# Kernel tuning notes

Measured on AMD Instinct MI355X. Metric: run time of the kernel, lower is better.

The kernel has to match this reference:

```python
import jax, jax.numpy as jnp
import numpy as np
import math
from jax import lax

B, T, D, K, H, MLP_DIM, WIN = 4, 2048, 1024, 64, 4, 4096, 128
KH = K // H          # eigenstates per head
HD = D // H          # attention head dim


def layer_norm(x, g, b, eps=1e-5):
    mu = jnp.mean(x, axis=-1, keepdims=True)
    var = jnp.mean(jnp.square(x - mu), axis=-1, keepdims=True)
    return (x - mu) * lax.rsqrt(var + eps) * g + b


def setup_inputs() -> dict:
    key = jax.random.key(0)
    ks = jax.random.split(key, 16)
    s = 0.02
    # layer_idx=1, n_layers=6 -> depth_ratio=0.2, decay_center=-1.7
    return {
        "x": jax.random.normal(ks[0], (B, T, D), jnp.float32),
        "prev_eigenstates": jax.random.normal(ks[1], (B, T, 2 * K), jnp.float32),
        "norm1_g": jnp.ones((D,), jnp.float32),
        "norm1_b": jnp.zeros((D,), jnp.float32),
        "in_proj_w": jax.random.normal(ks[2], (2 * K, D), jnp.float32) * s,
        "memory_gate": jnp.array(-3.0, jnp.float32),
        "memory_proj_w": jnp.eye(2 * K, dtype=jnp.float32),
        "log_decay": jax.random.uniform(ks[3], (K,), jnp.float32, -2.7, -1.2),
        "frequency": jnp.linspace(0.0, 2 * math.pi * (1 - 1 / K), K, dtype=jnp.float32),
        "coupling": jnp.tile(jnp.eye(KH, dtype=jnp.float32), (H, 1, 1))
                    + 0.01 * jax.random.normal(ks[4], (H, KH, KH), jnp.float32) / math.sqrt(KH),
        "main_gate_w": jax.random.normal(ks[5], (D, D), jnp.float32) * s,
        "main_gate_b": jnp.full((D,), -2.0, jnp.float32),
        "out_proj_w": jax.random.normal(ks[6], (D, 2 * K), jnp.float32) * s,
        "attn_norm_g": jnp.ones((D,), jnp.float32),
        "attn_norm_b": jnp.zeros((D,), jnp.float32),
        "attn_in_w": jax.random.normal(ks[7], (3 * D, D), jnp.float32) * s,
        "attn_in_b": jnp.zeros((3 * D,), jnp.float32),
        "attn_out_w": jax.random.normal(ks[8], (D, D), jnp.float32) * s,
        "attn_out_b": jnp.zeros((D,), jnp.float32),
        "norm2_g": jnp.ones((D,), jnp.float32),
        "norm2_b": jnp.zeros((D,), jnp.float32),
        "mlp_w1": jax.random.normal(ks[9], (MLP_DIM, D), jnp.float32) * s,
        "mlp_b1": jnp.zeros((MLP_DIM,), jnp.float32),
        "mlp_w2": jax.random.normal(ks[10], (D, MLP_DIM), jnp.float32) * s,
        "mlp_b2": jnp.zeros((D,), jnp.float32),
    }


def eigenstate_fft(log_decay, frequency, beta_r, beta_i):
    # diagonal complex SSM recurrence: c_t = lam * c_{t-1} + beta_t
    lam = jnp.exp(log_decay)
    lr = lam * jnp.cos(frequency)   # (K,)
    li = lam * jnp.sin(frequency)
    br = jnp.transpose(beta_r, (1, 0, 2))  # (T,B,K)
    bi = jnp.transpose(beta_i, (1, 0, 2))

    def step(carry, inp):
        sr, si = carry
        xr, xi = inp
        nr = lr * sr - li * si + xr
        ni = lr * si + li * sr + xi
        return (nr, ni), (nr, ni)

    init = (jnp.zeros(br.shape[1:], br.dtype), jnp.zeros(bi.shape[1:], bi.dtype))
    _, (cr, ci) = lax.scan(step, init, (br, bi))
    return jnp.transpose(cr, (1, 0, 2)), jnp.transpose(ci, (1, 0, 2))


def reference(x, prev_eigenstates, norm1_g, norm1_b, in_proj_w, memory_gate,
              memory_proj_w, log_decay, frequency, coupling, main_gate_w,
              main_gate_b, out_proj_w, attn_norm_g, attn_norm_b, attn_in_w,
              attn_in_b, attn_out_w, attn_out_b, norm2_g, norm2_b,
              mlp_w1, mlp_b1, mlp_w2, mlp_b2):
    b, t, d = x.shape
    residual = x
    x_norm = layer_norm(x, norm1_g, norm1_b)

    beta = jnp.einsum('btd,kd->btk', x_norm, in_proj_w)        # (B,T,2K)
    beta_r, beta_i = jnp.split(beta, 2, axis=-1)

    # cross-layer memory
    mg = jax.nn.sigmoid(memory_gate)
    prev = jnp.einsum('btk,jk->btj', prev_eigenstates, memory_proj_w)
    pr, pi = jnp.split(prev, 2, axis=-1)
    beta_r = beta_r + mg * pr
    beta_i = beta_i + mg * pi

    c_r, c_i = eigenstate_fft(log_decay, frequency, beta_r, beta_i)  # (B,T,K)

    # per-head coupling
    c_r_h = c_r.reshape(b, t, H, KH)
    c_i_h = c_i.reshape(b, t, H, KH)
    c_r = jnp.einsum('hjk,bthk->bthj', coupling, c_r_h).reshape(b, t, K)
    c_i = jnp.einsum('hjk,bthk->bthj', coupling, c_i_h).reshape(b, t, K)
    eigenstates_out = jnp.concatenate([c_r, c_i], axis=-1)     # (B,T,2K)

    h = jnp.einsum('btk,dk->btd', eigenstates_out, out_proj_w)
    # spectral gate (band gates computed in torch are unused in the output)
    main_g = jax.nn.sigmoid(jnp.einsum('btd,ed->bte', x_norm, main_gate_w) + main_gate_b)
    h = main_g * h
    x = residual + h

    # sliding-window attention (dense masked MHA, as in the source)
    attn_in = layer_norm(x, attn_norm_g, attn_norm_b)
    qkv = jnp.einsum('btd,ed->bte', attn_in, attn_in_w) + attn_in_b
    q, k_, v = jnp.split(qkv, 3, axis=-1)
    q = q.reshape(b, t, H, HD).transpose(0, 2, 1, 3)           # (B,H,T,hd)
    k_ = k_.reshape(b, t, H, HD).transpose(0, 2, 1, 3)
    v = v.reshape(b, t, H, HD).transpose(0, 2, 1, 3)
    scale = 1.0 / math.sqrt(HD)
    scores = jnp.einsum('bhqd,bhkd->bhqk', q, k_) * scale
    idx = jnp.arange(t)
    diff = idx[:, None] - idx[None, :]
    allowed = (diff >= 0) & (diff <= WIN)                      # True = attend
    scores = jnp.where(allowed, scores, jnp.finfo(scores.dtype).min)
    attn = jax.nn.softmax(scores, axis=-1)
    ao = jnp.einsum('bhqk,bhkd->bhqd', attn, v)
    ao = ao.transpose(0, 2, 1, 3).reshape(b, t, d)
    ao = jnp.einsum('btd,ed->bte', ao, attn_out_w) + attn_out_b
    x = x + ao

    # MLP
    x2 = layer_norm(x, norm2_g, norm2_b)
    m = jax.nn.silu(jnp.einsum('btd,md->btm', x2, mlp_w1) + mlp_b1)
    m = jnp.einsum('btm,dm->btd', m, mlp_w2) + mlp_b2
    x = x + m
    return (x, eigenstates_out)
```

## Files before the change

kernel.cpp:

```cpp
#include <hip/hip_runtime.h>


typedef __bf16 bf16_t;
typedef bf16_t bf16x8 __attribute__((ext_vector_type(8)));
typedef bf16_t bf16x4 __attribute__((ext_vector_type(4)));
typedef float  f32x4  __attribute__((ext_vector_type(4)));

#define Tc   2048
#define Dc   1024
#define BTc  8192
#define K2c  128
#define MLPc 4096

struct ConvSeg { const float* src; bf16_t* dst; int n; };
struct ConvArgs { ConvSeg s[9]; };

__global__ __launch_bounds__(256) void convert_kernel(ConvArgs a) {
    ConvSeg sg = a.s[blockIdx.y];
    int i = (blockIdx.x * 256 + threadIdx.x) * 4;
    if (i >= sg.n) return;
    float4 v = *(const float4*)(sg.src + i);
    bf16x4 o;
    o[0] = (bf16_t)v.x; o[1] = (bf16_t)v.y; o[2] = (bf16_t)v.z; o[3] = (bf16_t)v.w;
    *(bf16x4*)(sg.dst + i) = o;
}

__global__ __launch_bounds__(256) void ln_kernel(const float* __restrict__ x,
                                                 const float* __restrict__ g,
                                                 const float* __restrict__ bb,
                                                 bf16_t* __restrict__ out) {
    int row = blockIdx.x;
    int tid = threadIdx.x;
    float4 v = ((const float4*)(x + (size_t)row * Dc))[tid];
    float s  = v.x + v.y + v.z + v.w;
    float ss = v.x * v.x + v.y * v.y + v.z * v.z + v.w * v.w;
#pragma unroll
    for (int d = 32; d > 0; d >>= 1) {
        s  += __shfl_down(s, d);
        ss += __shfl_down(ss, d);
    }
    __shared__ float red[8];
    int wv = tid >> 6;
    if ((tid & 63) == 0) { red[wv] = s; red[4 + wv] = ss; }
    __syncthreads();
    s  = red[0] + red[1] + red[2] + red[3];
    ss = red[4] + red[5] + red[6] + red[7];
    float mean = s * (1.0f / Dc);
    float var  = ss * (1.0f / Dc) - mean * mean;
    float rstd = rsqrtf(var + 1e-5f);
    float4 g4 = ((const float4*)g)[tid];
    float4 b4 = ((const float4*)bb)[tid];
    bf16x4 o;
    o[0] = (bf16_t)((v.x - mean) * rstd * g4.x + b4.x);
    o[1] = (bf16_t)((v.y - mean) * rstd * g4.y + b4.y);
    o[2] = (bf16_t)((v.z - mean) * rstd * g4.z + b4.z);
    o[3] = (bf16_t)((v.w - mean) * rstd * g4.w + b4.w);
    *(bf16x4*)(out + (size_t)row * Dc + tid * 4) = o;
}

#define BM 128
#define BN 128
#define BK 32

struct EpiParams {
    const float* bias;
    float*       fout;
    const float* fin;
    bf16_t*      bout;
    bf16_t*      q; bf16_t* k; bf16_t* v;
    const float* hbuf;
};

#define GLOAD_LDS(g, l)                                                        \
    __builtin_amdgcn_global_load_lds(                                          \
        (const __attribute__((address_space(1))) unsigned int*)(g),            \
        (__attribute__((address_space(3))) unsigned int*)(l), 16, 0, 0)

template <int EPI>
__global__ __launch_bounds__(256) void gemm_tiled(const bf16_t* __restrict__ A,
                                                  const bf16_t* __restrict__ W,
                                                  int M, int N, int K,
                                                  EpiParams ep) {
    __shared__ bf16_t As[BM * BK];
    __shared__ bf16_t Bs[BN * BK];

    int tid = threadIdx.x;
    int wv = tid >> 6, lane = tid & 63;
    int lane16 = lane & 15, quad = lane >> 4;
    int nbn = N / BN;
    int bm = blockIdx.x / nbn, bn = blockIdx.x % nbn;
    int m0 = bm * BM, n0 = bn * BN;
    int wm = (wv >> 1) * 64, wn = (wv & 1) * 64;

    int lrow = lane >> 2;
    int lcol = (lane & 3) * 8;
    const bf16_t* ga = A + (size_t)(m0 + wv * 16 + lrow) * K + lcol;
    const bf16_t* gb = W + (size_t)(n0 + wv * 16 + lrow) * K + lcol;
    size_t gstep64 = (size_t)64 * K;
    bf16_t* la0 = &As[(wv * 16) * BK];
    bf16_t* la1 = &As[(64 + wv * 16) * BK];
    bf16_t* lb0 = &Bs[(wv * 16) * BK];
    bf16_t* lb1 = &Bs[(64 + wv * 16) * BK];

    f32x4 zz = {0.f, 0.f, 0.f, 0.f};
    f32x4 acc[4][4];
#pragma unroll
    for (int mi = 0; mi < 4; mi++)
#pragma unroll
        for (int ni = 0; ni < 4; ni++) acc[mi][ni] = zz;

    for (int k0 = 0; k0 < K; k0 += BK) {
        GLOAD_LDS(ga + k0, la0);
        GLOAD_LDS(ga + k0 + gstep64, la1);
        GLOAD_LDS(gb + k0, lb0);
        GLOAD_LDS(gb + k0 + gstep64, lb1);
        __syncthreads();
        bf16x8 af[4], bfr[4];
#pragma unroll
        for (int mi = 0; mi < 4; mi++)
            af[mi] = *(const bf16x8*)&As[(wm + mi * 16 + lane16) * BK + quad * 8];
#pragma unroll
        for (int ni = 0; ni < 4; ni++)
            bfr[ni] = *(const bf16x8*)&Bs[(wn + ni * 16 + lane16) * BK + quad * 8];
#pragma unroll
        for (int mi = 0; mi < 4; mi++)
#pragma unroll
            for (int ni = 0; ni < 4; ni++)
                acc[mi][ni] = __builtin_amdgcn_mfma_f32_16x16x32_bf16(
                    af[mi], bfr[ni], acc[mi][ni], 0, 0, 0);
        __syncthreads();
    }

#pragma unroll
    for (int mi = 0; mi < 4; mi++)
#pragma unroll
        for (int ni = 0; ni < 4; ni++)
#pragma unroll
            for (int r = 0; r < 4; r++) {
                int row = m0 + wm + mi * 16 + quad * 4 + r;
                int col = n0 + wn + ni * 16 + lane16;
                float v = acc[mi][ni][r];
                if constexpr (EPI == 0) {
                    ep.fout[(size_t)row * N + col] = v;
                } else if constexpr (EPI == 1) {
                    v += ep.bias[col];
                    ep.bout[(size_t)row * N + col] = (bf16_t)(v / (1.0f + __expf(-v)));
                } else if constexpr (EPI == 2) {
                    size_t o = (size_t)row * N + col;
                    ep.fout[o] = ep.fin[o] + v + ep.bias[col];
                } else if constexpr (EPI == 3) {
                    v += ep.bias[col];
                    int part = col >> 10, d1 = col & 1023;
                    int hh = d1 >> 8, hd = d1 & 255;
                    int b = row >> 11, t = row & 2047;
                    bf16_t* dst = (part == 0) ? ep.q : ep.k;
                    dst[(((size_t)(b * 4 + hh) * Tc + t) << 8) + hd] = (bf16_t)v;
                } else if constexpr (EPI == 4) {
                    size_t o = (size_t)row * N + col;
                    float g = 1.0f / (1.0f + __expf(-(v + ep.bias[col])));
                    ep.fout[o] = ep.fin[o] + g * ep.hbuf[o];
                } else if constexpr (EPI == 5) {
                    v += ep.bias[2048 + row];
                    int b = col >> 11, t = col & 2047;
                    int hh = row >> 8, dd = row & 255;
                    ep.v[((size_t)((b * 4 + hh) * 256 + dd)) * Tc + t] = (bf16_t)v;
                }
            }
}

__device__ __forceinline__ void mm32(const bf16_t* __restrict__ A,
                                     const bf16_t* __restrict__ W,
                                     int K, int m0, int n0,
                                     int lane16, int quad, f32x4 (&acc)[2][2]) {
    const bf16_t* a0 = A + (size_t)(m0 + lane16) * K + quad * 8;
    const bf16_t* a1 = a0 + (size_t)16 * K;
    const bf16_t* w0 = W + (size_t)(n0 + lane16) * K + quad * 8;
    const bf16_t* w1 = w0 + (size_t)16 * K;
#pragma unroll 4
    for (int k = 0; k < K; k += 32) {
        bf16x8 av0 = *(const bf16x8*)(a0 + k);
        bf16x8 av1 = *(const bf16x8*)(a1 + k);
        bf16x8 bv0 = *(const bf16x8*)(w0 + k);
        bf16x8 bv1 = *(const bf16x8*)(w1 + k);
        acc[0][0] = __builtin_amdgcn_mfma_f32_16x16x32_bf16(av0, bv0, acc[0][0], 0, 0, 0);
        acc[0][1] = __builtin_amdgcn_mfma_f32_16x16x32_bf16(av0, bv1, acc[0][1], 0, 0, 0);
        acc[1][0] = __builtin_amdgcn_mfma_f32_16x16x32_bf16(av1, bv0, acc[1][0], 0, 0, 0);
        acc[1][1] = __builtin_amdgcn_mfma_f32_16x16x32_bf16(av1, bv1, acc[1][1], 0, 0, 0);
    }
}

__global__ __launch_bounds__(256) void gemm_beta(const bf16_t* __restrict__ xn,
                                                 const bf16_t* __restrict__ ipw,
                                                 const bf16_t* __restrict__ prevb,
                                                 const bf16_t* __restrict__ mpw,
                                                 const float* __restrict__ mgate_p,
                                                 float* __restrict__ beta_c) {
    int lane = threadIdx.x & 63;
    int wave = threadIdx.x >> 6;
    int gid  = blockIdx.x * 4 + wave;
    int mt = gid / 4, nt = gid % 4;
    int m0 = mt * 32, n0 = nt * 32;
    int lane16 = lane & 15, quad = lane >> 4;
    f32x4 zz = {0.f, 0.f, 0.f, 0.f};
    f32x4 acc[2][2] = {{zz, zz}, {zz, zz}};
    mm32(xn, ipw, Dc, m0, n0, lane16, quad, acc);
    f32x4 acc2[2][2] = {{zz, zz}, {zz, zz}};
    mm32(prevb, mpw, K2c, m0, n0, lane16, quad, acc2);
    float mg = 1.0f / (1.0f + __expf(-mgate_p[0]));
    for (int mi = 0; mi < 2; mi++)
        for (int ni = 0; ni < 2; ni++)
            for (int r = 0; r < 4; r++) {
                int row = m0 + mi * 16 + quad * 4 + r;
                int col = n0 + ni * 16 + lane16;
                int b = row >> 11, t = row & 2047;
                beta_c[((size_t)b * K2c + col) * Tc + t] =
                    acc[mi][ni][r] + mg * acc2[mi][ni][r];
            }
}

__global__ __launch_bounds__(64) void scan_kernel(const float* __restrict__ beta_c,
                                                  const float* __restrict__ log_decay,
                                                  const float* __restrict__ freq,
                                                  float* __restrict__ cbuf) {
    int b = blockIdx.x >> 6;
    int k = blockIdx.x & 63;
    int lane = threadIdx.x;
    float lam = expf(log_decay[k]);
    float fr = freq[k];
    float lr = lam * cosf(fr), li = lam * sinf(fr);

    const float* br_p = beta_c + ((size_t)b * K2c + k) * Tc + lane * 32;
    const float* bi_p = beta_c + ((size_t)b * K2c + 64 + k) * Tc + lane * 32;
    float br[32], bi[32];
#pragma unroll
    for (int i = 0; i < 8; i++) {
        *(float4*)(&br[i * 4]) = ((const float4*)br_p)[i];
        *(float4*)(&bi[i * 4]) = ((const float4*)bi_p)[i];
    }
    float sr = 0.f, si = 0.f;
#pragma unroll
    for (int i = 0; i < 32; i++) {
        float nr = lr * sr - li * si + br[i];
        float ni = lr * si + li * sr + bi[i];
        sr = nr; si = ni;
    }
    float Mr = lr, Mi = li;
#pragma unroll
    for (int i = 0; i < 5; i++) {
        float nr = Mr * Mr - Mi * Mi, ni = 2.f * Mr * Mi;
        Mr = nr; Mi = ni;
    }
    float ir = sr, ii = si;
#pragma unroll
    for (int d = 1; d < 64; d <<= 1) {
        float pr = __shfl_up(ir, d);
        float pi = __shfl_up(ii, d);
        if (lane >= d) {
            ir += Mr * pr - Mi * pi;
            ii += Mr * pi + Mi * pr;
        }
        float nr = Mr * Mr - Mi * Mi, ni = 2.f * Mr * Mi;
        Mr = nr; Mi = ni;
    }
    float cr = __shfl_up(ir, 1), ci = __shfl_up(ii, 1);
    if (lane == 0) { cr = 0.f; ci = 0.f; }
    float* cr_p = cbuf + ((size_t)b * K2c + k) * Tc + lane * 32;
    float* ci_p = cbuf + ((size_t)b * K2c + 64 + k) * Tc + lane * 32;
    sr = cr; si = ci;
#pragma unroll
    for (int i = 0; i < 32; i++) {
        float nr = lr * sr - li * si + br[i];
        float ni = lr * si + li * sr + bi[i];
        sr = nr; si = ni;
        cr_p[i] = sr; ci_p[i] = si;
    }
}

__global__ __launch_bounds__(256) void coupling_kernel(const float* __restrict__ cbuf,
                                                       const float* __restrict__ cpl,
                                                       float* __restrict__ eig_out,
                                                       bf16_t* __restrict__ eigb) {
    int idx = blockIdx.x * 256 + threadIdx.x;
    int col = idx & 127;
    int t = (idx >> 7) & 2047;
    int b = idx >> 18;
    int ri = col >> 6, hj = col & 63, h2 = hj >> 4, j = hj & 15;
    const float* crow = cbuf + ((size_t)b * K2c + ri * 64 + h2 * 16) * Tc + t;
    const float* cw = cpl + (h2 * 16 + j) * 16;
    float acc = 0.f;
#pragma unroll
    for (int kk = 0; kk < 16; kk++) acc += cw[kk] * crow[(size_t)kk * Tc];
    eig_out[idx] = acc;
    eigb[idx] = (bf16_t)acc;
}

#define LDP 168

__global__ __launch_bounds__(256) void attn_mfma(const bf16_t* __restrict__ qb,
                                                 const bf16_t* __restrict__ kb,
                                                 const bf16_t* __restrict__ vt,
                                                 bf16_t* __restrict__ ao) {
    __shared__ bf16_t Pl[4 * 16 * LDP];
    int tid = threadIdx.x;
    int wv = tid >> 6, lane = tid & 63;
    int lane16 = lane & 15, quad = lane >> 4;
    int qblk = blockIdx.x & 31;
    int bh = blockIdx.x >> 5;
    int qw0 = qblk * 64 + wv * 16;
    const bf16_t* qp = qb + (size_t)bh * Tc * 256;
    const bf16_t* kp = kb + (size_t)bh * Tc * 256;
    const bf16_t* vp = vt + (size_t)bh * 256 * Tc;
    bf16_t* Pw = &Pl[wv * 16 * LDP];

    for (int i = lane; i < 16 * 24; i += 64) {
        int r = i / 24, c = 144 + (i % 24);
        Pw[r * LDP + c] = (bf16_t)0.f;
    }

    bf16x8 qf[8];
#pragma unroll
    for (int ks = 0; ks < 8; ks++)
        qf[ks] = *(const bf16x8*)(qp + (size_t)(qw0 + lane16) * 256 + ks * 32 + quad * 8);

    f32x4 zz = {0.f, 0.f, 0.f, 0.f};
    f32x4 S[9];
#pragma unroll
    for (int jt = 0; jt < 9; jt++) S[jt] = zz;
    int kbase = qw0 - 128;

#pragma unroll
    for (int ks = 0; ks < 8; ks++) {
        bf16x8 kf[9];
#pragma unroll
        for (int jt = 0; jt < 9; jt++) {
            int krow = kbase + jt * 16 + lane16;
            krow = krow < 0 ? 0 : krow;
            kf[jt] = *(const bf16x8*)(kp + (size_t)krow * 256 + ks * 32 + quad * 8);
        }
#pragma unroll
        for (int jt = 0; jt < 9; jt++)
            S[jt] = __builtin_amdgcn_mfma_f32_16x16x32_bf16(qf[ks], kf[jt], S[jt], 0, 0, 0);
    }

    float m[4], l[4];
#pragma unroll
    for (int r = 0; r < 4; r++) m[r] = -1e30f;
#pragma unroll
    for (int jt = 0; jt < 9; jt++) {
        int kg = kbase + jt * 16 + lane16;
#pragma unroll
        for (int r = 0; r < 4; r++) {
            int qrow = qw0 + quad * 4 + r;
            bool ok = (kg >= 0) && (kg <= qrow) && (kg >= qrow - 128);
            float v = ok ? S[jt][r] * 0.0625f : -1e30f;
            S[jt][r] = v;
            m[r] = fmaxf(m[r], v);
        }
    }
#pragma unroll
    for (int d = 1; d < 16; d <<= 1)
#pragma unroll
        for (int r = 0; r < 4; r++)
            m[r] = fmaxf(m[r], __shfl_xor(m[r], d));
#pragma unroll
    for (int r = 0; r < 4; r++) l[r] = 0.f;
#pragma unroll
    for (int jt = 0; jt < 9; jt++)
#pragma unroll
        for (int r = 0; r < 4; r++) {
            float p = __expf(S[jt][r] - m[r]);
            S[jt][r] = p;
            l[r] += p;
        }
#pragma unroll
    for (int d = 1; d < 16; d <<= 1)
#pragma unroll
        for (int r = 0; r < 4; r++)
            l[r] += __shfl_xor(l[r], d);

#pragma unroll
    for (int jt = 0; jt < 9; jt++)
#pragma unroll
        for (int r = 0; r < 4; r++)
            Pw[(quad * 4 + r) * LDP + jt * 16 + lane16] = (bf16_t)S[jt][r];
    __syncthreads();

    f32x4 O[16];
#pragma unroll
    for (int nt = 0; nt < 16; nt++) O[nt] = zz;
#pragma unroll
    for (int ks = 0; ks < 5; ks++) {
        bf16x8 pf = *(const bf16x8*)&Pw[lane16 * LDP + ks * 32 + quad * 8];
        int kidx = kbase + ks * 32 + quad * 8;
        kidx = kidx < 0 ? 0 : kidx;
        kidx = kidx > (Tc - 8) ? (Tc - 8) : kidx;
#pragma unroll
        for (int nt = 0; nt < 16; nt++) {
            bf16x8 vf = *(const bf16x8*)(vp + (size_t)(nt * 16 + lane16) * Tc + kidx);
            O[nt] = __builtin_amdgcn_mfma_f32_16x16x32_bf16(pf, vf, O[nt], 0, 0, 0);
        }
    }

    float rl[4];
#pragma unroll
    for (int r = 0; r < 4; r++) rl[r] = 1.0f / l[r];
    int b = bh >> 2, h = bh & 3;
#pragma unroll
    for (int nt = 0; nt < 16; nt++)
#pragma unroll
        for (int r = 0; r < 4; r++) {
            int qrow = qw0 + quad * 4 + r;
            int dim = nt * 16 + lane16;
            ao[((size_t)(b * Tc + qrow)) * Dc + h * 256 + dim] = (bf16_t)(O[nt][r] * rl[r]);
        }
}

extern "C" void kernel_launch(void* const* d_in, const int* in_sizes, int n_in,
                              void* d_out, int out_size, void* d_ws, size_t ws_size,
                              hipStream_t stream) {
    const float* x            = (const float*)d_in[0];
    const float* prev_eig     = (const float*)d_in[1];
    const float* norm1_g      = (const float*)d_in[2];
    const float* norm1_b      = (const float*)d_in[3];
    const float* in_proj_w    = (const float*)d_in[4];
    const float* memory_gate  = (const float*)d_in[5];
    const float* memory_proj_w= (const float*)d_in[6];
    const float* log_decay    = (const float*)d_in[7];
    const float* frequency    = (const float*)d_in[8];
    const float* coupling     = (const float*)d_in[9];
    const float* main_gate_w  = (const float*)d_in[10];
    const float* main_gate_b  = (const float*)d_in[11];
    const float* out_proj_w   = (const float*)d_in[12];
    const float* attn_norm_g  = (const float*)d_in[13];
    const float* attn_norm_b  = (const float*)d_in[14];
    const float* attn_in_w    = (const float*)d_in[15];
    const float* attn_in_b    = (const float*)d_in[16];
    const float* attn_out_w   = (const float*)d_in[17];
    const float* attn_out_b   = (const float*)d_in[18];
    const float* norm2_g      = (const float*)d_in[19];
    const float* norm2_b      = (const float*)d_in[20];
    const float* mlp_w1       = (const float*)d_in[21];
    const float* mlp_b1       = (const float*)d_in[22];
    const float* mlp_w2       = (const float*)d_in[23];
    const float* mlp_b2       = (const float*)d_in[24];

    char* ws = (char*)d_ws;
    bf16_t* ipw_b  = (bf16_t*)(ws + 0);
    bf16_t* mpw_b  = (bf16_t*)(ws + 262144);
    bf16_t* mgw_b  = (bf16_t*)(ws + 294912);
    bf16_t* opw_b  = (bf16_t*)(ws + 2392064);
    bf16_t* aiw_b  = (bf16_t*)(ws + 2654208);
    bf16_t* aow_b  = (bf16_t*)(ws + 8945664);
    bf16_t* w1_b   = (bf16_t*)(ws + 11042816);
    bf16_t* w2_b   = (bf16_t*)(ws + 19431424);
    bf16_t* prev_b = (bf16_t*)(ws + 27820032);
    const size_t OFF_ACTA = 29917184;
    const size_t OFF_BIG  = OFF_ACTA + 16777216;
    bf16_t* actA   = (bf16_t*)(ws + OFF_ACTA);
    float*  beta_c = (float*)(ws + OFF_BIG);
    float*  cbuf   = (float*)(ws + OFF_BIG + 4194304);
    bf16_t* eigb   = (bf16_t*)(ws + OFF_BIG + 8388608);
    float*  hbuf   = (float*)(ws + OFF_BIG + 16777216);
    bf16_t* qbuf   = (bf16_t*)(ws + OFF_BIG);
    bf16_t* kbuf   = (bf16_t*)(ws + OFF_BIG + 16777216);
    bf16_t* vtbuf  = (bf16_t*)(ws + OFF_BIG + 33554432);
    bf16_t* mbuf   = (bf16_t*)(ws + OFF_BIG);

    float* out_x   = (float*)d_out;
    float* out_eig = out_x + (size_t)BTc * Dc;
    float* xres    = out_x;

    ConvArgs ca;
    ca.s[0] = ConvSeg{in_proj_w,     ipw_b,  131072};
    ca.s[1] = ConvSeg{memory_proj_w, mpw_b,  16384};
    ca.s[2] = ConvSeg{main_gate_w,   mgw_b,  1048576};
    ca.s[3] = ConvSeg{out_proj_w,    opw_b,  131072};
    ca.s[4] = ConvSeg{attn_in_w,     aiw_b,  3145728};
    ca.s[5] = ConvSeg{attn_out_w,    aow_b,  1048576};
    ca.s[6] = ConvSeg{mlp_w1,        w1_b,   4194304};
    ca.s[7] = ConvSeg{mlp_w2,        w2_b,   4194304};
    ca.s[8] = ConvSeg{prev_eig,      prev_b, 1048576};
    convert_kernel<<<dim3(4096, 9), 256, 0, stream>>>(ca);

    EpiParams ep{};

    ln_kernel<<<BTc, 256, 0, stream>>>(x, norm1_g, norm1_b, actA);
    gemm_beta<<<256, 256, 0, stream>>>(actA, ipw_b, prev_b, mpw_b, memory_gate, beta_c);
    scan_kernel<<<256, 64, 0, stream>>>(beta_c, log_decay, frequency, cbuf);
    coupling_kernel<<<4096, 256, 0, stream>>>(cbuf, coupling, out_eig, eigb);
    ep = EpiParams{}; ep.fout = hbuf;
    gemm_tiled<0><<<(BTc/BM)*(Dc/BN), 256, 0, stream>>>(eigb, opw_b, BTc, Dc, K2c, ep);
    ep = EpiParams{}; ep.bias = main_gate_b; ep.fin = x; ep.fout = xres; ep.hbuf = hbuf;
    gemm_tiled<4><<<(BTc/BM)*(Dc/BN), 256, 0, stream>>>(actA, mgw_b, BTc, Dc, Dc, ep);
    ln_kernel<<<BTc, 256, 0, stream>>>(xres, attn_norm_g, attn_norm_b, actA);
    ep = EpiParams{}; ep.bias = attn_in_b; ep.q = qbuf; ep.k = kbuf;
    gemm_tiled<3><<<(BTc/BM)*(2048/BN), 256, 0, stream>>>(actA, aiw_b, BTc, 2048, Dc, ep);
    ep = EpiParams{}; ep.bias = attn_in_b; ep.v = vtbuf;
    gemm_tiled<5><<<(Dc/BM)*(BTc/BN), 256, 0, stream>>>(aiw_b + (size_t)2048 * Dc, actA,
                                                        Dc, BTc, Dc, ep);
    attn_mfma<<<512, 256, 0, stream>>>(qbuf, kbuf, vtbuf, actA);
    ep = EpiParams{}; ep.bias = attn_out_b; ep.fin = xres; ep.fout = xres;
    gemm_tiled<2><<<(BTc/BM)*(Dc/BN), 256, 0, stream>>>(actA, aow_b, BTc, Dc, Dc, ep);
    ln_kernel<<<BTc, 256, 0, stream>>>(xres, norm2_g, norm2_b, actA);
    ep = EpiParams{}; ep.bias = mlp_b1; ep.bout = mbuf;
    gemm_tiled<1><<<(BTc/BM)*(MLPc/BN), 256, 0, stream>>>(actA, w1_b, BTc, MLPc, Dc, ep);
    ep = EpiParams{}; ep.bias = mlp_b2; ep.fin = xres; ep.fout = out_x;
    gemm_tiled<2><<<(BTc/BM)*(Dc/BN), 256, 0, stream>>>(mbuf, w2_b, BTc, Dc, MLPc, ep);

    (void)in_sizes; (void)n_in; (void)out_size; (void)ws_size;
}
```

Measured before the change: 695.1 us.

## Fuse out_proj GEMM into main-gate GEMM and XOR-swizzle LDS tile layout

The out_proj GEMM (K=128) is folded into the main-gate GEMM kernel as a second accumulator pass, so the fp32 intermediate h buffer is never written to or read from global memory and one launch goes away. Separately, the LDS tile layout in gemm_tiled is XOR-swizzled on the column chunk to reduce bank conflicts on the MFMA fragment reads, which affects every GEMM. The fused kernel holds a second 4x4 accumulator set, raising register pressure and possibly lowering occupancy.

```diff
diff --git a/kernel.cpp b/kernel.cpp
--- a/kernel.cpp
+++ b/kernel.cpp
@@ -68,7 +68,7 @@
     const float* fin;
     bf16_t*      bout;
     bf16_t*      q; bf16_t* k; bf16_t* v;
-    const float* hbuf;
+    const bf16_t* a2; const bf16_t* w2;
 };
 
 #define GLOAD_LDS(g, l)                                                        \
@@ -93,7 +93,7 @@
     int wm = (wv >> 1) * 64, wn = (wv & 1) * 64;
 
     int lrow = lane >> 2;
-    int lcol = (lane & 3) * 8;
+    int lcol = (((lane & 3) ^ ((lrow >> 1) & 3))) * 8;
     const bf16_t* ga = A + (size_t)(m0 + wv * 16 + lrow) * K + lcol;
     const bf16_t* gb = W + (size_t)(n0 + wv * 16 + lrow) * K + lcol;
     size_t gstep64 = (size_t)64 * K;
@@ -102,6 +102,8 @@
     bf16_t* lb0 = &Bs[(wv * 16) * BK];
     bf16_t* lb1 = &Bs[(64 + wv * 16) * BK];
 
+    int pc = (quad ^ ((lane16 >> 1) & 3)) * 8;
+
     f32x4 zz = {0.f, 0.f, 0.f, 0.f};
     f32x4 acc[4][4];
 #pragma unroll
@@ -118,10 +120,10 @@
         bf16x8 af[4], bfr[4];
 #pragma unroll
         for (int mi = 0; mi < 4; mi++)
-            af[mi] = *(const bf16x8*)&As[(wm + mi * 16 + lane16) * BK + quad * 8];
+            af[mi] = *(const bf16x8*)&As[(wm + mi * 16 + lane16) * BK + pc];
 #pragma unroll
         for (int ni = 0; ni < 4; ni++)
-            bfr[ni] = *(const bf16x8*)&Bs[(wn + ni * 16 + lane16) * BK + quad * 8];
+            bfr[ni] = *(const bf16x8*)&Bs[(wn + ni * 16 + lane16) * BK + pc];
 #pragma unroll
         for (int mi = 0; mi < 4; mi++)
 #pragma unroll
@@ -131,6 +133,38 @@
         __syncthreads();
     }
 
+    f32x4 acc2[4][4];
+    if constexpr (EPI == 6) {
+#pragma unroll
+        for (int mi = 0; mi < 4; mi++)
+#pragma unroll
+            for (int ni = 0; ni < 4; ni++) acc2[mi][ni] = zz;
+        const bf16_t* ga2 = ep.a2 + (size_t)(m0 + wv * 16 + lrow) * K2c + lcol;
+        const bf16_t* gb2 = ep.w2 + (size_t)(n0 + wv * 16 + lrow) * K2c + lcol;
+        size_t gstep64b = (size_t)64 * K2c;
+        for (int k0 = 0; k0 < K2c; k0 += BK) {
+            GLOAD_LDS(ga2 + k0, la0);
+            GLOAD_LDS(ga2 + k0 + gstep64b, la1);
+            GLOAD_LDS(gb2 + k0, lb0);
+            GLOAD_LDS(gb2 + k0 + gstep64b, lb1);
+            __syncthreads();
+            bf16x8 af[4], bfr[4];
+#pragma unroll
+            for (int mi = 0; mi < 4; mi++)
+                af[mi] = *(const bf16x8*)&As[(wm + mi * 16 + lane16) * BK + pc];
+#pragma unroll
+            for (int ni = 0; ni < 4; ni++)
+                bfr[ni] = *(const bf16x8*)&Bs[(wn + ni * 16 + lane16) * BK + pc];
+#pragma unroll
+            for (int mi = 0; mi < 4; mi++)
+#pragma unroll
+                for (int ni = 0; ni < 4; ni++)
+                    acc2[mi][ni] = __builtin_amdgcn_mfma_f32_16x16x32_bf16(
+                        af[mi], bfr[ni], acc2[mi][ni], 0, 0, 0);
+            __syncthreads();
+        }
+    }
+
 #pragma unroll
     for (int mi = 0; mi < 4; mi++)
 #pragma unroll
@@ -140,9 +174,7 @@
                 int row = m0 + wm + mi * 16 + quad * 4 + r;
                 int col = n0 + wn + ni * 16 + lane16;
                 float v = acc[mi][ni][r];
-                if constexpr (EPI == 0) {
-                    ep.fout[(size_t)row * N + col] = v;
-                } else if constexpr (EPI == 1) {
+                if constexpr (EPI == 1) {
                     v += ep.bias[col];
                     ep.bout[(size_t)row * N + col] = (bf16_t)(v / (1.0f + __expf(-v)));
                 } else if constexpr (EPI == 2) {
@@ -155,15 +187,15 @@
                     int b = row >> 11, t = row & 2047;
                     bf16_t* dst = (part == 0) ? ep.q : ep.k;
                     dst[(((size_t)(b * 4 + hh) * Tc + t) << 8) + hd] = (bf16_t)v;
-                } else if constexpr (EPI == 4) {
-                    size_t o = (size_t)row * N + col;
-                    float g = 1.0f / (1.0f + __expf(-(v + ep.bias[col])));
-                    ep.fout[o] = ep.fin[o] + g * ep.hbuf[o];
                 } else if constexpr (EPI == 5) {
                     v += ep.bias[2048 + row];
                     int b = col >> 11, t = col & 2047;
                     int hh = row >> 8, dd = row & 255;
                     ep.v[((size_t)((b * 4 + hh) * 256 + dd)) * Tc + t] = (bf16_t)v;
+                } else if constexpr (EPI == 6) {
+                    size_t o = (size_t)row * N + col;
+                    float g = 1.0f / (1.0f + __expf(-(v + ep.bias[col])));
+                    ep.fout[o] = ep.fin[o] + g * acc2[mi][ni][r];
                 }
             }
 }
@@ -460,7 +492,6 @@
     float*  beta_c = (float*)(ws + OFF_BIG);
     float*  cbuf   = (float*)(ws + OFF_BIG + 4194304);
     bf16_t* eigb   = (bf16_t*)(ws + OFF_BIG + 8388608);
-    float*  hbuf   = (float*)(ws + OFF_BIG + 16777216);
     bf16_t* qbuf   = (bf16_t*)(ws + OFF_BIG);
     bf16_t* kbuf   = (bf16_t*)(ws + OFF_BIG + 16777216);
     bf16_t* vtbuf  = (bf16_t*)(ws + OFF_BIG + 33554432);
@@ -488,10 +519,9 @@
     gemm_beta<<<256, 256, 0, stream>>>(actA, ipw_b, prev_b, mpw_b, memory_gate, beta_c);
     scan_kernel<<<256, 64, 0, stream>>>(beta_c, log_decay, frequency, cbuf);
     coupling_kernel<<<4096, 256, 0, stream>>>(cbuf, coupling, out_eig, eigb);
-    ep = EpiParams{}; ep.fout = hbuf;
-    gemm_tiled<0><<<(BTc/BM)*(Dc/BN), 256, 0, stream>>>(eigb, opw_b, BTc, Dc, K2c, ep);
-    ep = EpiParams{}; ep.bias = main_gate_b; ep.fin = x; ep.fout = xres; ep.hbuf = hbuf;
-    gemm_tiled<4><<<(BTc/BM)*(Dc/BN), 256, 0, stream>>>(actA, mgw_b, BTc, Dc, Dc, ep);
+    ep = EpiParams{}; ep.bias = main_gate_b; ep.fin = x; ep.fout = xres;
+    ep.a2 = eigb; ep.w2 = opw_b;
+    gemm_tiled<6><<<(BTc/BM)*(Dc/BN), 256, 0, stream>>>(actA, mgw_b, BTc, Dc, Dc, ep);
     ln_kernel<<<BTc, 256, 0, stream>>>(xres, attn_norm_g, attn_norm_b, actA);
     ep = EpiParams{}; ep.bias = attn_in_b; ep.q = qbuf; ep.k = kbuf;
     gemm_tiled<3><<<(BTc/BM)*(2048/BN), 256, 0, stream>>>(actA, aiw_b, BTc, 2048, Dc, ep);
```

New measurement: 699.2 us. No clear change (+0.6%).
